# Performance work log

Measured on AMD Instinct MI355X. Metric: run time of the kernel, lower is better.

## Reference

```python
import jax, jax.numpy as jnp
import numpy as np

SCALE = 32 ** (-0.5)  # hardcoded in the original module, independent of head_size

def setup_inputs() -> dict:
    key = jax.random.key(0)
    k1, k2, k3, k4 = jax.random.split(key, 4)
    B, T, E, H = 8, 4096, 2048, 128
    x = jax.random.normal(k1, (B, T, E), dtype=jnp.float32)
    Wq = jax.random.normal(k2, (E, H), dtype=jnp.float32) * (E ** -0.5)
    Wk = jax.random.normal(k3, (E, H), dtype=jnp.float32) * (E ** -0.5)
    Wv = jax.random.normal(k4, (E, H), dtype=jnp.float32) * (E ** -0.5)
    return {"x": x, "Wq": Wq, "Wk": Wk, "Wv": Wv}

def reference(x, Wq, Wk, Wv):
    # q,k,v: [B,T,H]
    q = jnp.einsum('bte,eh->bth', x, Wq)
    k = jnp.einsum('bte,eh->bth', x, Wk)
    v = jnp.einsum('bte,eh->bth', x, Wv)
    # wei: [B, T(query), T(key)]
    wei = jnp.einsum('bqh,bkh->bqk', q, k) * SCALE
    # NOTE: original uses F.softmax(wei, dim=1) -> normalize over the QUERY axis
    wei = jax.nn.softmax(wei, axis=1)
    # dropout prob is 0 in this deterministic baseline (eval mode)
    out = jnp.einsum('bqk,bkh->bqh', wei, v)
    return out
```

## Files before the change

kernel.cpp:

```cpp
#include <hip/hip_runtime.h>
#include <hip/hip_bf16.h>
#include <hip/hip_fp16.h>

#define Bn 8
#define Tn 4096
#define En 2048
#define Hn 128

typedef __attribute__((ext_vector_type(8))) short bf16x8;
typedef __attribute__((ext_vector_type(4))) float f32x4;
typedef __attribute__((ext_vector_type(4))) unsigned int u32x4;

typedef const __attribute__((address_space(1))) unsigned int* gptr_t;
typedef __attribute__((address_space(3))) unsigned int* lptr_t;

static __device__ __forceinline__ void gload16(const void* g, void* l) {
    __builtin_amdgcn_global_load_lds((gptr_t)g, (lptr_t)l, 16, 0, 0);
}

static __device__ __forceinline__ unsigned short f2bf(float f) {
    union { float f; unsigned u; } v; v.f = f;
    unsigned r = v.u + 0x7FFFu + ((v.u >> 16) & 1u);
    return (unsigned short)(r >> 16);
}
static __device__ __forceinline__ float b2f(unsigned short bits) {
    union { unsigned u; float f; } v; v.u = ((unsigned)bits) << 16;
    return v.f;
}
static __device__ __forceinline__ unsigned cvtpk(float lo, float hi) {
    unsigned r;
    asm volatile("v_cvt_pk_bf16_f32 %0, %1, %2" : "=v"(r) : "v"(lo), "v"(hi));
    return r;
}

#define MFMA16(a, b, c) __builtin_amdgcn_mfma_f32_16x16x32_bf16((a), (b), (c), 0, 0, 0)
#define EXP2F(x) __builtin_amdgcn_exp2f(x)
#define WAIT_VM_PUB(N) do { asm volatile("s_waitcnt vmcnt(" #N ")" ::: "memory"); \
                            __builtin_amdgcn_sched_barrier(0); \
                            __builtin_amdgcn_s_barrier(); \
                            __builtin_amdgcn_sched_barrier(0); } while (0)
#define LGKM_BARRIER() do { asm volatile("s_waitcnt lgkmcnt(0)" ::: "memory"); \
                            __builtin_amdgcn_s_barrier(); \
                            __builtin_amdgcn_sched_barrier(0); } while (0)

__global__ __launch_bounds__(256) void prep_w(const float* __restrict__ Wq,
                                              const float* __restrict__ Wk,
                                              const float* __restrict__ Wv,
                                              unsigned short* __restrict__ Wt) {
    int idx = blockIdx.x * 256 + threadIdx.x;
    int w = idx / (En * Hn);
    int rem = idx - w * (En * Hn);
    int kx = rem >> 7;
    int n  = rem & 127;
    const float* W = (w == 0) ? Wq : (w == 1) ? Wk : Wv;
    float f = W[rem];
    if (w == 0) f *= (0.17677669529663687f * 1.4426950408889634f);
    Wt[(size_t)w * En * Hn + (size_t)n * En + kx] = f2bf(f);
}

__global__ __launch_bounds__(256, 3) void qkv_mfma(const float* __restrict__ x,
                                                   const unsigned short* __restrict__ Wt,
                                                   unsigned short* __restrict__ qs,
                                                   unsigned short* __restrict__ ks,
                                                   unsigned short* __restrict__ vT) {
    __shared__ __align__(16) float Al[128][64];
    __shared__ __align__(16) unsigned short Bl[128][64];
    const int bid = blockIdx.x;
    const int w = bid % 3;
    const int m0 = (bid / 3) * 128;
    const int b = m0 >> 12;
    const int tb = m0 & (Tn - 1);
    const int t = threadIdx.x;
    const int lane = t & 63, wid = t >> 6;
    const int wr = (wid >> 1) * 64, wc = (wid & 1) * 64;
    const int fr = lane & 15, fq = lane >> 4;
    const unsigned short* Wb = Wt + (size_t)w * En * Hn;
    const int aR = lane >> 4, aC = lane & 15;
    const int bR = lane >> 3, bC = lane & 7;

    f32x4 acc[4][4] = {};
    for (int k0 = 0; k0 < En; k0 += 64) {
        __syncthreads();
        #pragma unroll
        for (int s = 0; s < 8; ++s) {
            int seg = wid * 8 + s;
            int r = seg * 4 + aR;
            gload16(&x[(size_t)(m0 + r) * En + k0 + ((aC ^ (r & 15)) * 4)],
                    (char*)Al + seg * 1024 + lane * 16);
        }
        #pragma unroll
        for (int s = 0; s < 4; ++s) {
            int seg = wid * 4 + s;
            int r = seg * 8 + bR;
            gload16(&Wb[(size_t)r * En + k0 + ((bC ^ (r & 7)) * 8)],
                    (char*)Bl + seg * 1024 + lane * 16);
        }
        __syncthreads();
        #pragma unroll
        for (int ksub = 0; ksub < 2; ++ksub) {
            bf16x8 av[4], bv[4];
            #pragma unroll
            for (int mi = 0; mi < 4; ++mi) {
                int row = wr + mi * 16 + fr;
                const char* base = (const char*)Al + row * 256;
                int c0 = ksub * 8 + fq * 2;
                f32x4 a0 = *(const f32x4*)(base + ((c0 ^ (row & 15)) << 4));
                f32x4 a1 = *(const f32x4*)(base + (((c0 + 1) ^ (row & 15)) << 4));
                u32x4 pk;
                pk[0] = cvtpk(a0[0], a0[1]);
                pk[1] = cvtpk(a0[2], a0[3]);
                pk[2] = cvtpk(a1[0], a1[1]);
                pk[3] = cvtpk(a1[2], a1[3]);
                av[mi] = *reinterpret_cast<bf16x8*>(&pk);
            }
            #pragma unroll
            for (int ni = 0; ni < 4; ++ni) {
                int row = wc + ni * 16 + fr;
                int ch = (ksub * 4 + fq) ^ (row & 7);
                bv[ni] = *reinterpret_cast<const bf16x8*>((const char*)Bl + row * 128 + ch * 16);
            }
            #pragma unroll
            for (int mi = 0; mi < 4; ++mi)
                #pragma unroll
                for (int ni = 0; ni < 4; ++ni)
                    acc[mi][ni] = MFMA16(av[mi], bv[ni], acc[mi][ni]);
        }
    }

    if (w < 2) {
        unsigned short* out = (w == 0) ? qs : ks;
        #pragma unroll
        for (int mi = 0; mi < 4; ++mi)
            #pragma unroll
            for (int ni = 0; ni < 4; ++ni)
                #pragma unroll
                for (int r = 0; r < 4; ++r) {
                    int row = m0 + wr + mi * 16 + fq * 4 + r;
                    int col = wc + ni * 16 + fr;
                    out[(size_t)row * Hn + col] = f2bf(acc[mi][ni][r]);
                }
    } else {
        #pragma unroll
        for (int mi = 0; mi < 4; ++mi)
            #pragma unroll
            for (int ni = 0; ni < 4; ++ni)
                #pragma unroll
                for (int r = 0; r < 4; ++r) {
                    int tt = tb + wr + mi * 16 + fq * 4 + r;
                    int h  = wc + ni * 16 + fr;
                    vT[((size_t)b * Hn + h) * Tn + tt] = f2bf(acc[mi][ni][r]);
                }
    }
}

__global__ __launch_bounds__(256, 2) void stats_qk(const unsigned short* __restrict__ qs,
                                                   const unsigned short* __restrict__ ks,
                                                   float2* __restrict__ part) {
    __shared__ __align__(16) char smem[65536];
    const int bid = blockIdx.x;
    const int b = bid & 7;
    const int rest = bid >> 3;
    const int kt = rest & 31;
    const int qh = rest >> 5;
    const int k0 = kt * 128;
    const unsigned short* qb = qs + (size_t)b * Tn * Hn;
    const unsigned short* kb = ks + (size_t)b * Tn * Hn;
    const int t = threadIdx.x;
    const int lane = t & 63, wid = t >> 6;
    const int wk = wid >> 1, wq = wid & 1;
    const int fr = lane & 15, fq = lane >> 4;
    const int srow = t >> 4, schk = t & 15;

    #pragma unroll
    for (int it = 0; it < 8; ++it) {
        int r = it * 16 + srow;
        gload16(&kb[(size_t)(k0 + r) * Hn + ((schk ^ (r & 15)) * 8)],
                smem + it * 4096 + t * 16);
    }
    #pragma unroll
    for (int it = 0; it < 4; ++it) {
        int r = it * 16 + srow;
        gload16(&qb[(size_t)(qh * 2048 + r) * Hn + ((schk ^ (r & 15)) * 8)],
                smem + 32768 + it * 4096 + t * 16);
    }
    __syncthreads();
    bf16x8 av[4][4];
    #pragma unroll
    for (int mi = 0; mi < 4; ++mi)
        #pragma unroll
        for (int kc = 0; kc < 4; ++kc) {
            int row = wk * 64 + mi * 16 + fr;
            int ch = (kc * 4 + fq) ^ (row & 15);
            av[mi][kc] = *reinterpret_cast<const bf16x8*>(smem + row * 256 + ch * 16);
        }

    float m[4][4], l[4][4];
    #pragma unroll
    for (int mi = 0; mi < 4; ++mi)
        #pragma unroll
        for (int r = 0; r < 4; ++r) { m[mi][r] = -INFINITY; l[mi][r] = 0.f; }

    for (int step = 0; step < 32; ++step) {
        const int cur = step & 1;
        const int qn = qh * 2048 + ((step + 1) & 31) * 64;
        #pragma unroll
        for (int it = 0; it < 4; ++it) {
            int r = it * 16 + srow;
            gload16(&qb[(size_t)(qn + r) * Hn + ((schk ^ (r & 15)) * 8)],
                    smem + 32768 + (cur ^ 1) * 16384 + it * 4096 + t * 16);
        }
        WAIT_VM_PUB(4);
        const char* Qc = smem + 32768 + cur * 16384;
        f32x4 acc[4][2] = {};
        __builtin_amdgcn_s_setprio(1);
        #pragma unroll
        for (int kc = 0; kc < 4; ++kc) {
            bf16x8 bv[2];
            #pragma unroll
            for (int ni = 0; ni < 2; ++ni) {
                int row = wq * 32 + ni * 16 + fr;
                int ch = (kc * 4 + fq) ^ (row & 15);
                bv[ni] = *reinterpret_cast<const bf16x8*>(Qc + row * 256 + ch * 16);
            }
            #pragma unroll
            for (int mi = 0; mi < 4; ++mi)
                #pragma unroll
                for (int ni = 0; ni < 2; ++ni)
                    acc[mi][ni] = MFMA16(av[mi][kc], bv[ni], acc[mi][ni]);
        }
        __builtin_amdgcn_s_setprio(0);
        #pragma unroll
        for (int mi = 0; mi < 4; ++mi)
            #pragma unroll
            for (int r = 0; r < 4; ++r) {
                float v0 = acc[mi][0][r], v1 = acc[mi][1][r];
                float mn = fmaxf(m[mi][r], fmaxf(v0, v1));
                l[mi][r] = l[mi][r] * EXP2F(m[mi][r] - mn) + EXP2F(v0 - mn) + EXP2F(v1 - mn);
                m[mi][r] = mn;
            }
        LGKM_BARRIER();
    }
    #pragma unroll
    for (int off = 1; off <= 8; off <<= 1) {
        #pragma unroll
        for (int mi = 0; mi < 4; ++mi)
            #pragma unroll
            for (int r = 0; r < 4; ++r) {
                float mo = __shfl_xor(m[mi][r], off);
                float lo = __shfl_xor(l[mi][r], off);
                float mn = fmaxf(m[mi][r], mo);
                l[mi][r] = l[mi][r] * EXP2F(m[mi][r] - mn) + lo * EXP2F(mo - mn);
                m[mi][r] = mn;
            }
    }
    if (fr == 0) {
        #pragma unroll
        for (int mi = 0; mi < 4; ++mi)
            #pragma unroll
            for (int r = 0; r < 4; ++r) {
                int k = k0 + wk * 64 + mi * 16 + fq * 4 + r;
                part[((size_t)b * Tn + k) * 4 + qh * 2 + wq] = make_float2(m[mi][r], l[mi][r]);
            }
    }
}

__global__ __launch_bounds__(256) void stats_comb(const float2* __restrict__ part,
                                                  float* __restrict__ mr) {
    int g = blockIdx.x * 256 + threadIdx.x;
    const float2* pp = part + (size_t)g * 4;
    float2 p0 = pp[0], p1 = pp[1], p2 = pp[2], p3 = pp[3];
    float M = fmaxf(fmaxf(p0.x, p1.x), fmaxf(p2.x, p3.x));
    float L = p0.y * EXP2F(p0.x - M) + p1.y * EXP2F(p1.x - M) +
              p2.y * EXP2F(p2.x - M) + p3.y * EXP2F(p3.x - M);
    mr[g] = M + __log2f(L);
}

__global__ __launch_bounds__(256) void scale_v(const unsigned short* __restrict__ vT,
                                               const float* __restrict__ mr,
                                               unsigned short* __restrict__ vn) {
    size_t i = ((size_t)blockIdx.x * 256 + threadIdx.x) * 8;
    int t0 = (int)(i & (Tn - 1));
    int b = (int)(i >> 19);
    const float* mrb = mr + (size_t)b * Tn + t0;
    ushort4 v0 = *reinterpret_cast<const ushort4*>(vT + i);
    ushort4 v1 = *reinterpret_cast<const ushort4*>(vT + i + 4);
    float4 s0 = *reinterpret_cast<const float4*>(mrb);
    float4 s1 = *reinterpret_cast<const float4*>(mrb + 4);
    unsigned o[4];
    o[0] = cvtpk(b2f(v0.x) * EXP2F(-s0.x), b2f(v0.y) * EXP2F(-s0.y));
    o[1] = cvtpk(b2f(v0.z) * EXP2F(-s0.z), b2f(v0.w) * EXP2F(-s0.w));
    o[2] = cvtpk(b2f(v1.x) * EXP2F(-s1.x), b2f(v1.y) * EXP2F(-s1.y));
    o[3] = cvtpk(b2f(v1.z) * EXP2F(-s1.z), b2f(v1.w) * EXP2F(-s1.w));
    *reinterpret_cast<u32x4*>(vn + i) = *reinterpret_cast<u32x4*>(o);
}

__global__ __launch_bounds__(256, 2) void attn_pv(const unsigned short* __restrict__ qs,
                                                  const unsigned short* __restrict__ ks,
                                                  const unsigned short* __restrict__ vn,
                                                  float* __restrict__ opart) {
    __shared__ __align__(16) char smem[81920];
    const int bid = blockIdx.x;
    const int b = bid & 7;
    const int rest = bid >> 3;
    const int qp = rest & 31;
    const int kh = rest >> 5;
    const int kbase = kh * 2048;
    const unsigned short* qg = qs + (size_t)b * Tn * Hn;
    const unsigned short* kg = ks + (size_t)b * Tn * Hn;
    const unsigned short* vg = vn + (size_t)b * Hn * Tn;
    const int t = threadIdx.x;
    const int lane = t & 63, wid = t >> 6;
    const int wk = wid >> 1, wq = wid & 1;
    const int fr = lane & 15, fq = lane >> 4;
    const int srow16 = t >> 4, schk16 = t & 15;
    const int srow8 = t >> 3, schk8 = t & 7;

    bf16x8 bq[2][2][4];
    #pragma unroll
    for (int qt = 0; qt < 2; ++qt) {
        int qb0 = qp * 64 + qt * 2048;
        #pragma unroll
        for (int ni = 0; ni < 2; ++ni)
            #pragma unroll
            for (int kc = 0; kc < 4; ++kc) {
                int row = qb0 + wq * 32 + ni * 16 + fr;
                bq[qt][ni][kc] = *reinterpret_cast<const bf16x8*>(
                    &qg[(size_t)row * Hn + kc * 32 + fq * 8]);
            }
    }
    #pragma unroll
    for (int it = 0; it < 4; ++it) {
        int r = it * 16 + srow16;
        gload16(&kg[(size_t)(kbase + r) * Hn + ((schk16 ^ (r & 15)) * 8)],
                smem + it * 4096 + t * 16);
        int rv = it * 32 + srow8;
        gload16(&vg[(size_t)rv * Tn + kbase + ((schk8 ^ (rv & 7)) * 8)],
                smem + 32768 + it * 4096 + t * 16);
    }
    __syncthreads();

    f32x4 acc_o[2][4][2] = {};
    for (int s = 0; s < 32; ++s) {
        const int cur = s & 1;
        {
            const int knr = kbase + ((s + 1) & 31) * 64;
            #pragma unroll
            for (int it = 0; it < 4; ++it) {
                int r = it * 16 + srow16;
                gload16(&kg[(size_t)(knr + r) * Hn + ((schk16 ^ (r & 15)) * 8)],
                        smem + (cur ^ 1) * 16384 + it * 4096 + t * 16);
                int rv = it * 32 + srow8;
                gload16(&vg[(size_t)rv * Tn + knr + ((schk8 ^ (rv & 7)) * 8)],
                        smem + 32768 + (cur ^ 1) * 16384 + it * 4096 + t * 16);
            }
        }
        WAIT_VM_PUB(8);
        const char* Kc = smem + cur * 16384;
        #pragma unroll
        for (int qt = 0; qt < 2; ++qt) {
            char* Pb = smem + 65536 + qt * 8192;
            f32x4 acc_s[2][2] = {};
            __builtin_amdgcn_s_setprio(1);
            #pragma unroll
            for (int kc = 0; kc < 4; ++kc) {
                bf16x8 avk[2];
                #pragma unroll
                for (int mi = 0; mi < 2; ++mi) {
                    int row = wk * 32 + mi * 16 + fr;
                    int ch = (kc * 4 + fq) ^ (row & 15);
                    avk[mi] = *reinterpret_cast<const bf16x8*>(Kc + row * 256 + ch * 16);
                }
                #pragma unroll
                for (int mi = 0; mi < 2; ++mi)
                    #pragma unroll
                    for (int ni = 0; ni < 2; ++ni)
                        acc_s[mi][ni] = MFMA16(avk[mi], bq[qt][ni][kc], acc_s[mi][ni]);
            }
            __builtin_amdgcn_s_setprio(0);
            #pragma unroll
            for (int mi = 0; mi < 2; ++mi)
                #pragma unroll
                for (int ni = 0; ni < 2; ++ni) {
                    float e0 = EXP2F(acc_s[mi][ni][0]);
                    float e1 = EXP2F(acc_s[mi][ni][1]);
                    float e2 = EXP2F(acc_s[mi][ni][2]);
                    float e3 = EXP2F(acc_s[mi][ni][3]);
                    int q = wq * 32 + ni * 16 + fr;
                    int chunk = (wk * 4 + mi * 2 + (fq >> 1)) ^ (q & 7);
                    *reinterpret_cast<uint2*>(Pb + q * 128 + chunk * 16 + (fq & 1) * 8) =
                        make_uint2(cvtpk(e0, e1), cvtpk(e2, e3));
                }
        }
        LGKM_BARRIER();
        const char* Vc = smem + 32768 + cur * 16384;
        __builtin_amdgcn_s_setprio(1);
        #pragma unroll
        for (int kc = 0; kc < 2; ++kc) {
            bf16x8 bp[2][2];
            #pragma unroll
            for (int qt = 0; qt < 2; ++qt)
                #pragma unroll
                for (int ni = 0; ni < 2; ++ni) {
                    int qrow = wq * 32 + ni * 16 + fr;
                    int ch = (kc * 4 + fq) ^ (qrow & 7);
                    bp[qt][ni] = *reinterpret_cast<const bf16x8*>(
                        smem + 65536 + qt * 8192 + qrow * 128 + ch * 16);
                }
            #pragma unroll
            for (int mi = 0; mi < 4; ++mi) {
                int row = wk * 64 + mi * 16 + fr;
                int ch = (kc * 4 + fq) ^ (row & 7);
                bf16x8 avv = *reinterpret_cast<const bf16x8*>(Vc + row * 128 + ch * 16);
                #pragma unroll
                for (int qt = 0; qt < 2; ++qt)
                    #pragma unroll
                    for (int ni = 0; ni < 2; ++ni)
                        acc_o[qt][mi][ni] = MFMA16(avv, bp[qt][ni], acc_o[qt][mi][ni]);
            }
        }
        __builtin_amdgcn_s_setprio(0);
        LGKM_BARRIER();
    }

    float* Ol = (float*)smem;
    __syncthreads();
    float* op = opart + (size_t)kh * Bn * Tn * Hn + (size_t)b * Tn * Hn;
    #pragma unroll
    for (int qt = 0; qt < 2; ++qt) {
        #pragma unroll
        for (int mi = 0; mi < 4; ++mi)
            #pragma unroll
            for (int ni = 0; ni < 2; ++ni) {
                int q = wq * 32 + ni * 16 + fr;
                int h = wk * 64 + mi * 16 + fq * 4;
                *reinterpret_cast<float4*>(&Ol[q * 132 + h]) =
                    make_float4(acc_o[qt][mi][ni][0], acc_o[qt][mi][ni][1],
                                acc_o[qt][mi][ni][2], acc_o[qt][mi][ni][3]);
            }
        __syncthreads();
        int qrow0 = qp * 64 + qt * 2048;
        #pragma unroll
        for (int j = 0; j < 8; ++j) {
            int idx = j * 256 + t;
            int row = idx >> 5, c = (idx & 31) * 4;
            *reinterpret_cast<float4*>(&op[(size_t)(qrow0 + row) * Hn + c]) =
                *reinterpret_cast<const float4*>(&Ol[row * 132 + c]);
        }
        __syncthreads();
    }
}

__global__ __launch_bounds__(256) void combine(const float* __restrict__ opart,
                                               float* __restrict__ out) {
    size_t i = ((size_t)blockIdx.x * 256 + threadIdx.x) * 4;
    const size_t half = (size_t)Bn * Tn * Hn;
    float4 a = *reinterpret_cast<const float4*>(opart + i);
    float4 b = *reinterpret_cast<const float4*>(opart + half + i);
    *reinterpret_cast<float4*>(out + i) =
        make_float4(a.x + b.x, a.y + b.y, a.z + b.z, a.w + b.w);
}

extern "C" void kernel_launch(void* const* d_in, const int* in_sizes, int n_in,
                              void* d_out, int out_size, void* d_ws, size_t ws_size,
                              hipStream_t stream) {
    const float* x  = (const float*)d_in[0];
    const float* Wq = (const float*)d_in[1];
    const float* Wk = (const float*)d_in[2];
    const float* Wv = (const float*)d_in[3];
    float* out = (float*)d_out;

    char* p = (char*)d_ws;
    unsigned short* qs = (unsigned short*)p; p += (size_t)Bn * Tn * Hn * 2;
    unsigned short* ks = (unsigned short*)p; p += (size_t)Bn * Tn * Hn * 2;
    unsigned short* vT = (unsigned short*)p; p += (size_t)Bn * Tn * Hn * 2;
    unsigned short* vn = (unsigned short*)p; p += (size_t)Bn * Tn * Hn * 2;
    unsigned short* Wt = (unsigned short*)p; p += (size_t)3 * En * Hn * 2;
    float2* part       = (float2*)p;         p += (size_t)Bn * Tn * 4 * sizeof(float2);
    float* mr          = (float*)p;          p += (size_t)Bn * Tn * sizeof(float);
    float* opart       = (float*)p;          p += (size_t)2 * Bn * Tn * Hn * sizeof(float);
    size_t needed = (size_t)(p - (char*)d_ws);
    if (ws_size < needed) return;

    prep_w<<<dim3(3 * En * Hn / 256), dim3(256), 0, stream>>>(Wq, Wk, Wv, Wt);
    qkv_mfma<<<dim3((Bn * Tn / 128) * 3), dim3(256), 0, stream>>>(x, Wt, qs, ks, vT);
    stats_qk<<<dim3(512), dim3(256), 0, stream>>>(qs, ks, part);
    stats_comb<<<dim3(Bn * Tn / 256), dim3(256), 0, stream>>>(part, mr);
    scale_v<<<dim3((size_t)Bn * Hn * Tn / (256 * 8)), dim3(256), 0, stream>>>(vT, mr, vn);
    attn_pv<<<dim3(512), dim3(256), 0, stream>>>(qs, ks, vn, opart);
    combine<<<dim3((size_t)Bn * Tn * Hn / (256 * 4)), dim3(256), 0, stream>>>(opart, out);
}
```

Measured before the change: 276.1 us.

## Double-buffer QKV projection tiles with register-staged bf16 conversion of x

The QKV projection GEMM now uses two LDS buffers. The next k-tile of x is loaded into registers and W is loaded straight to LDS while MFMAs run on the current tile. The fp32 x tile is converted to bf16 once, before being written to LDS with a new swizzle, so the per-fragment conversion inside the MFMA loop goes away and the A tile in LDS is half the size. The cost is higher register use from the staged float4s, and occupancy bounds drop from 3 to 2 blocks per CU. On the last iteration the loop also wraps around and loads an unused tile.

```diff
diff --git a/kernel.cpp b/kernel.cpp
--- a/kernel.cpp
+++ b/kernel.cpp
@@ -58,13 +58,13 @@
     Wt[(size_t)w * En * Hn + (size_t)n * En + kx] = f2bf(f);
 }
 
-__global__ __launch_bounds__(256, 3) void qkv_mfma(const float* __restrict__ x,
+__global__ __launch_bounds__(256, 2) void qkv_mfma(const float* __restrict__ x,
                                                    const unsigned short* __restrict__ Wt,
                                                    unsigned short* __restrict__ qs,
                                                    unsigned short* __restrict__ ks,
                                                    unsigned short* __restrict__ vT) {
-    __shared__ __align__(16) float Al[128][64];
-    __shared__ __align__(16) unsigned short Bl[128][64];
+    __shared__ __align__(16) unsigned short Al[2][128][64];
+    __shared__ __align__(16) unsigned short Bl[2][128][64];
     const int bid = blockIdx.x;
     const int w = bid % 3;
     const int m0 = (bid / 3) * 128;
@@ -75,49 +75,63 @@
     const int wr = (wid >> 1) * 64, wc = (wid & 1) * 64;
     const int fr = lane & 15, fq = lane >> 4;
     const unsigned short* Wb = Wt + (size_t)w * En * Hn;
-    const int aR = lane >> 4, aC = lane & 15;
+    const int agrp = t >> 4, aln = t & 15;
     const int bR = lane >> 3, bC = lane & 7;
 
+    #pragma unroll
+    for (int j = 0; j < 8; ++j) {
+        int row = agrp * 8 + j;
+        float4 v = *reinterpret_cast<const float4*>(&x[(size_t)(m0 + row) * En + aln * 4]);
+        int c = (aln >> 1) ^ ((row ^ (row >> 3)) & 7);
+        *reinterpret_cast<uint2*>((char*)&Al[0][0][0] + row * 128 + c * 16 + (aln & 1) * 8)
+            = make_uint2(cvtpk(v.x, v.y), cvtpk(v.z, v.w));
+    }
+    #pragma unroll
+    for (int s_ = 0; s_ < 4; ++s_) {
+        int seg = wid * 4 + s_;
+        int r = seg * 8 + bR;
+        gload16(&Wb[(size_t)r * En + ((bC ^ (r & 7)) * 8)],
+                (char*)&Bl[0][0][0] + seg * 1024 + lane * 16);
+    }
+    asm volatile("s_waitcnt vmcnt(0) lgkmcnt(0)" ::: "memory");
+    __builtin_amdgcn_s_barrier();
+    __builtin_amdgcn_sched_barrier(0);
+
     f32x4 acc[4][4] = {};
-    for (int k0 = 0; k0 < En; k0 += 64) {
-        __syncthreads();
-        #pragma unroll
-        for (int s = 0; s < 8; ++s) {
-            int seg = wid * 8 + s;
-            int r = seg * 4 + aR;
-            gload16(&x[(size_t)(m0 + r) * En + k0 + ((aC ^ (r & 15)) * 4)],
-                    (char*)Al + seg * 1024 + lane * 16);
-        }
-        #pragma unroll
-        for (int s = 0; s < 4; ++s) {
-            int seg = wid * 4 + s;
+    for (int s = 0; s < 32; ++s) {
+        const int cur = s & 1;
+        const int kn = ((s + 1) & 31) * 64;
+        float4 ar_[8];
+        #pragma unroll
+        for (int j = 0; j < 8; ++j) {
+            int row = agrp * 8 + j;
+            ar_[j] = *reinterpret_cast<const float4*>(&x[(size_t)(m0 + row) * En + kn + aln * 4]);
+        }
+        __builtin_amdgcn_sched_barrier(0);
+        #pragma unroll
+        for (int s_ = 0; s_ < 4; ++s_) {
+            int seg = wid * 4 + s_;
             int r = seg * 8 + bR;
-            gload16(&Wb[(size_t)r * En + k0 + ((bC ^ (r & 7)) * 8)],
-                    (char*)Bl + seg * 1024 + lane * 16);
-        }
-        __syncthreads();
+            gload16(&Wb[(size_t)r * En + kn + ((bC ^ (r & 7)) * 8)],
+                    (char*)&Bl[cur ^ 1][0][0] + seg * 1024 + lane * 16);
+        }
+        __builtin_amdgcn_sched_barrier(0);
         #pragma unroll
         for (int ksub = 0; ksub < 2; ++ksub) {
             bf16x8 av[4], bv[4];
             #pragma unroll
             for (int mi = 0; mi < 4; ++mi) {
                 int row = wr + mi * 16 + fr;
-                const char* base = (const char*)Al + row * 256;
-                int c0 = ksub * 8 + fq * 2;
-                f32x4 a0 = *(const f32x4*)(base + ((c0 ^ (row & 15)) << 4));
-                f32x4 a1 = *(const f32x4*)(base + (((c0 + 1) ^ (row & 15)) << 4));
-                u32x4 pk;
-                pk[0] = cvtpk(a0[0], a0[1]);
-                pk[1] = cvtpk(a0[2], a0[3]);
-                pk[2] = cvtpk(a1[0], a1[1]);
-                pk[3] = cvtpk(a1[2], a1[3]);
-                av[mi] = *reinterpret_cast<bf16x8*>(&pk);
+                int ch = (ksub * 4 + fq) ^ ((row ^ (row >> 3)) & 7);
+                av[mi] = *reinterpret_cast<const bf16x8*>(
+                    (const char*)&Al[cur][0][0] + row * 128 + ch * 16);
             }
             #pragma unroll
             for (int ni = 0; ni < 4; ++ni) {
                 int row = wc + ni * 16 + fr;
                 int ch = (ksub * 4 + fq) ^ (row & 7);
-                bv[ni] = *reinterpret_cast<const bf16x8*>((const char*)Bl + row * 128 + ch * 16);
+                bv[ni] = *reinterpret_cast<const bf16x8*>(
+                    (const char*)&Bl[cur][0][0] + row * 128 + ch * 16);
             }
             #pragma unroll
             for (int mi = 0; mi < 4; ++mi)
@@ -125,6 +139,18 @@
                 for (int ni = 0; ni < 4; ++ni)
                     acc[mi][ni] = MFMA16(av[mi], bv[ni], acc[mi][ni]);
         }
+        asm volatile("s_waitcnt vmcnt(4)" ::: "memory");
+        __builtin_amdgcn_sched_barrier(0);
+        #pragma unroll
+        for (int j = 0; j < 8; ++j) {
+            int row = agrp * 8 + j;
+            int c = (aln >> 1) ^ ((row ^ (row >> 3)) & 7);
+            *reinterpret_cast<uint2*>((char*)&Al[cur ^ 1][0][0] + row * 128 + c * 16 + (aln & 1) * 8)
+                = make_uint2(cvtpk(ar_[j].x, ar_[j].y), cvtpk(ar_[j].z, ar_[j].w));
+        }
+        asm volatile("s_waitcnt vmcnt(0) lgkmcnt(0)" ::: "memory");
+        __builtin_amdgcn_s_barrier();
+        __builtin_amdgcn_sched_barrier(0);
     }
 
     if (w < 2) {
```

Result: slower. 288.1 us (median of 3 runs) (+4.3%).
